# Optimization experiments

Measured on AMD Instinct MI355X. Metric: run time of the kernel, lower is better.

Reference implementation:

```python
import jax, jax.numpy as jnp
import numpy as np

S, B, D, H = 4096, 4, 1024, 16
DH = D // H


def _xavier(key, fan_in, fan_out):
    bound = float(np.sqrt(6.0 / (fan_in + fan_out)))
    return jax.random.uniform(key, (fan_out, fan_in), jnp.float32, -bound, bound)


def setup_inputs() -> dict:
    key = jax.random.key(0)
    kq, kk, kv, kwq, kwk, kwv = jax.random.split(key, 6)
    return {
        "q": jax.random.normal(kq, (S, B, D), jnp.float32),
        "k": jax.random.normal(kk, (S, B, D), jnp.float32),
        "v": jax.random.normal(kv, (S, B, D), jnp.float32),
        "Wq": _xavier(kwq, D, D),
        "Wk": _xavier(kwk, D, D),
        "Wv": _xavier(kwv, D, D),
    }


def reference(q, k, v, Wq, Wk, Wv):
    s, b = q.shape[:2]
    # exp feature maps after bias-free linear projections (nn.Linear: x @ W.T)
    q_h = jnp.exp(q @ Wq.T).reshape(s, b, H, DH)
    k_h = jnp.exp(k @ Wk.T).reshape(s, b, H, DH)
    v_h = (v @ Wv.T).reshape(s, b, H, DH)
    # original: einsum('sbnd,sbnde->sbne', q, k[...,None]*v[None...]) / same-with-ones
    # contract over d without materializing the (s,b,n,d,e) outer product
    qk = jnp.einsum('sbnd,sbnd->sbn', q_h, k_h)[..., None]  # (s,b,n,1)
    out = (qk * v_h) / qk                                   # (s,b,n,dh)
    out = out.reshape(s, b, D)
    return jnp.cumsum(out, axis=1)  # cumsum over dim=1 (batch), as in source
```

## Files before the change

### kernel.cpp

```cpp
#include <hip/hip_runtime.h>
#include <hip/hip_bf16.h>


typedef short s16x8 __attribute__((ext_vector_type(8)));
typedef float f32x4 __attribute__((ext_vector_type(4)));

constexpr int M_ = 16384, N_ = 1024, K_ = 1024;
constexpr int BM = 256, BN = 256, BK = 64;
constexpr int KT = K_ / BK;
constexpr int LDS_BUF = 65536;
constexpr size_t LDS_TOTAL = 131072;

static __device__ __forceinline__ unsigned cvtpk(float lo, float hi) {
  unsigned r;
  asm("v_cvt_pk_bf16_f32 %0, %1, %2" : "=v"(r) : "v"(lo), "v"(hi));
  return r;
}

__global__ __launch_bounds__(512, 2) void la_gemm_cumsum(
    const float* __restrict__ Vp,
    const float* __restrict__ Wp,
    float* __restrict__ out)
{
  extern __shared__ char lds[];

  const int tid  = threadIdx.x;
  const int lane = tid & 63;
  const int wave = tid >> 6;
  const int wr = wave >> 2;
  const int wc = wave & 3;

  const int gid = blockIdx.x;
  const int xcd = gid & 7;
  const int q   = gid >> 3;
  const int mt  = xcd * 8 + (q >> 2);
  const int nt  = q & 3;

  const int srow   = tid >> 3;
  const int schunk = tid & 7;
  const float* sAp = Vp + (size_t)(mt * 256 + srow) * K_ + schunk * 8;
  const float* sBp = Wp + (size_t)(nt * 256 + srow) * K_ + schunk * 8;
  const int wbyte = srow * 128 + ((schunk ^ (srow & 7)) << 4);

  const int basa0 = (wr * 128 + (lane & 15)) * 128 + (((lane >> 4) ^ (lane & 7)) << 4);
  const int basa1 = basa0 ^ 64;
  const int basb0 = (wc * 64 + (lane & 15)) * 128 + (((lane >> 4) ^ (lane & 7)) << 4);
  const int basb1 = basb0 ^ 64;

  f32x4 acc[8][4] = {};
  float4 sa[8], sb[8];

  auto loadset = [&](int kt) {
#pragma unroll
    for (int i = 0; i < 4; ++i) {
      const float* pa = sAp + kt * 64 + i * (64 * K_);
      const float* pb = sBp + kt * 64 + i * (64 * K_);
      sa[2 * i]     = *(const float4*)pa;
      sa[2 * i + 1] = *(const float4*)(pa + 4);
      sb[2 * i]     = *(const float4*)pb;
      sb[2 * i + 1] = *(const float4*)(pb + 4);
    }
  };

  auto cvtwrite = [&](int buf) {
    char* A = lds + buf * LDS_BUF;
    char* B = A + 32768;
#pragma unroll
    for (int i = 0; i < 4; ++i) {
      uint4 wa, wb;
      wa.x = cvtpk(sa[2*i].x,   sa[2*i].y);   wa.y = cvtpk(sa[2*i].z,   sa[2*i].w);
      wa.z = cvtpk(sa[2*i+1].x, sa[2*i+1].y); wa.w = cvtpk(sa[2*i+1].z, sa[2*i+1].w);
      wb.x = cvtpk(sb[2*i].x,   sb[2*i].y);   wb.y = cvtpk(sb[2*i].z,   sb[2*i].w);
      wb.z = cvtpk(sb[2*i+1].x, sb[2*i+1].y); wb.w = cvtpk(sb[2*i+1].z, sb[2*i+1].w);
      *(uint4*)(A + wbyte + i * 8192) = wa;
      *(uint4*)(B + wbyte + i * 8192) = wb;
    }
  };

  auto compute = [&](int buf) {
    const char* A = lds + buf * LDS_BUF;
    const char* B = A + 32768;
#pragma unroll
    for (int kk = 0; kk < 2; ++kk) {
      const int ba = kk ? basa1 : basa0;
      const int bb = kk ? basb1 : basb0;
      s16x8 bf[4];
#pragma unroll
      for (int n = 0; n < 4; ++n) bf[n] = *(const s16x8*)(B + bb + n * 2048);
#pragma unroll
      for (int mh = 0; mh < 2; ++mh) {
        s16x8 af[4];
#pragma unroll
        for (int m = 0; m < 4; ++m) af[m] = *(const s16x8*)(A + ba + (mh * 4 + m) * 2048);
        __builtin_amdgcn_s_setprio(1);
#pragma unroll
        for (int m = 0; m < 4; ++m)
#pragma unroll
          for (int n = 0; n < 4; ++n)
            acc[mh * 4 + m][n] =
                __builtin_amdgcn_mfma_f32_16x16x32_bf16(af[m], bf[n], acc[mh * 4 + m][n], 0, 0, 0);
        __builtin_amdgcn_s_setprio(0);
      }
    }
  };

  loadset(0);
  cvtwrite(0);
  __syncthreads();

  for (int kt = 0; kt < KT; ++kt) {
    const int cur = kt & 1;
    if (kt + 1 < KT) loadset(kt + 1);
    compute(cur);
    if (kt + 1 < KT) cvtwrite(cur ^ 1);
    __syncthreads();
  }

#pragma unroll
  for (int m = 0; m < 8; ++m) {
    const int row0 = mt * 256 + wr * 128 + m * 16 + ((lane >> 4) << 2);
#pragma unroll
    for (int n = 0; n < 4; ++n) {
      f32x4 a = acc[m][n];
      a.y += a.x;  a.z += a.y;  a.w += a.z;
      const int col = nt * 256 + wc * 64 + n * 16 + (lane & 15);
      out[(size_t)(row0 + 0) * N_ + col] = a.x;
      out[(size_t)(row0 + 1) * N_ + col] = a.y;
      out[(size_t)(row0 + 2) * N_ + col] = a.z;
      out[(size_t)(row0 + 3) * N_ + col] = a.w;
    }
  }
}

extern "C" void kernel_launch(void* const* d_in, const int* in_sizes, int n_in,
                              void* d_out, int out_size, void* d_ws, size_t ws_size,
                              hipStream_t stream) {
  const float* v  = (const float*)d_in[2];
  const float* Wv = (const float*)d_in[5];
  float* out = (float*)d_out;
  (void)d_ws; (void)ws_size; (void)in_sizes; (void)n_in; (void)out_size;

  static int attr_done = 0;
  hipFuncSetAttribute((const void*)la_gemm_cumsum,
                      hipFuncAttributeMaxDynamicSharedMemorySize, (int)LDS_TOTAL);
  (void)attr_done;

  la_gemm_cumsum<<<dim3(256), dim3(512), LDS_TOTAL, stream>>>(v, Wv, out);
}
```

Baseline: 50.25 us.

## Interleave global prefetch and LDS writes with MFMA phases using barrier gates

Splits each K-tile iteration into four phases. Each phase issues LDS fragment reads plus a slice of the next tile's global loads or bf16 conversion writes, then waits at a workgroup barrier before running 16 MFMAs. The intent is to spread memory traffic evenly across the compute so that global latency and LDS writes overlap with matrix math, instead of bunching all loads before compute and all writes after it. In exchange it adds several more s_barrier calls per iteration and forces lgkmcnt(0) waits, which could serialize the waves if the phases are not balanced.

```diff
diff --git a/kernel.cpp b/kernel.cpp
--- a/kernel.cpp
+++ b/kernel.cpp
@@ -43,77 +43,105 @@
   const int wbyte = srow * 128 + ((schunk ^ (srow & 7)) << 4);
 
   const int basa0 = (wr * 128 + (lane & 15)) * 128 + (((lane >> 4) ^ (lane & 7)) << 4);
-  const int basa1 = basa0 ^ 64;
   const int basb0 = (wc * 64 + (lane & 15)) * 128 + (((lane >> 4) ^ (lane & 7)) << 4);
-  const int basb1 = basb0 ^ 64;
 
   f32x4 acc[8][4] = {};
   float4 sa[8], sb[8];
 
-  auto loadset = [&](int kt) {
-#pragma unroll
-    for (int i = 0; i < 4; ++i) {
-      const float* pa = sAp + kt * 64 + i * (64 * K_);
-      const float* pb = sBp + kt * 64 + i * (64 * K_);
-      sa[2 * i]     = *(const float4*)pa;
-      sa[2 * i + 1] = *(const float4*)(pa + 4);
-      sb[2 * i]     = *(const float4*)pb;
-      sb[2 * i + 1] = *(const float4*)(pb + 4);
-    }
-  };
+#define LOADGRP(g, kt1) do {                                                  \
+    const float* pa_ = sAp + (kt1) * 64 + (g) * (64 * K_);                    \
+    const float* pb_ = sBp + (kt1) * 64 + (g) * (64 * K_);                    \
+    sa[2*(g)]   = *(const float4*)pa_;  sa[2*(g)+1] = *(const float4*)(pa_+4);\
+    sb[2*(g)]   = *(const float4*)pb_;  sb[2*(g)+1] = *(const float4*)(pb_+4);\
+  } while (0)
 
-  auto cvtwrite = [&](int buf) {
-    char* A = lds + buf * LDS_BUF;
-    char* B = A + 32768;
-#pragma unroll
-    for (int i = 0; i < 4; ++i) {
-      uint4 wa, wb;
-      wa.x = cvtpk(sa[2*i].x,   sa[2*i].y);   wa.y = cvtpk(sa[2*i].z,   sa[2*i].w);
-      wa.z = cvtpk(sa[2*i+1].x, sa[2*i+1].y); wa.w = cvtpk(sa[2*i+1].z, sa[2*i+1].w);
-      wb.x = cvtpk(sb[2*i].x,   sb[2*i].y);   wb.y = cvtpk(sb[2*i].z,   sb[2*i].w);
-      wb.z = cvtpk(sb[2*i+1].x, sb[2*i+1].y); wb.w = cvtpk(sb[2*i+1].z, sb[2*i+1].w);
-      *(uint4*)(A + wbyte + i * 8192) = wa;
-      *(uint4*)(B + wbyte + i * 8192) = wb;
-    }
-  };
+#define WRITEGRP(g, Aw, Bw) do {                                              \
+    uint4 wa_, wb_;                                                           \
+    wa_.x = cvtpk(sa[2*(g)].x,   sa[2*(g)].y);                                \
+    wa_.y = cvtpk(sa[2*(g)].z,   sa[2*(g)].w);                                \
+    wa_.z = cvtpk(sa[2*(g)+1].x, sa[2*(g)+1].y);                              \
+    wa_.w = cvtpk(sa[2*(g)+1].z, sa[2*(g)+1].w);                              \
+    wb_.x = cvtpk(sb[2*(g)].x,   sb[2*(g)].y);                                \
+    wb_.y = cvtpk(sb[2*(g)].z,   sb[2*(g)].w);                                \
+    wb_.z = cvtpk(sb[2*(g)+1].x, sb[2*(g)+1].y);                              \
+    wb_.w = cvtpk(sb[2*(g)+1].z, sb[2*(g)+1].w);                              \
+    *(uint4*)((Aw) + wbyte + (g) * 8192) = wa_;                               \
+    *(uint4*)((Bw) + wbyte + (g) * 8192) = wb_;                               \
+  } while (0)
 
-  auto compute = [&](int buf) {
-    const char* A = lds + buf * LDS_BUF;
-    const char* B = A + 32768;
-#pragma unroll
-    for (int kk = 0; kk < 2; ++kk) {
-      const int ba = kk ? basa1 : basa0;
-      const int bb = kk ? basb1 : basb0;
-      s16x8 bf[4];
-#pragma unroll
-      for (int n = 0; n < 4; ++n) bf[n] = *(const s16x8*)(B + bb + n * 2048);
-#pragma unroll
-      for (int mh = 0; mh < 2; ++mh) {
-        s16x8 af[4];
-#pragma unroll
-        for (int m = 0; m < 4; ++m) af[m] = *(const s16x8*)(A + ba + (mh * 4 + m) * 2048);
-        __builtin_amdgcn_s_setprio(1);
-#pragma unroll
-        for (int m = 0; m < 4; ++m)
-#pragma unroll
-          for (int n = 0; n < 4; ++n)
-            acc[mh * 4 + m][n] =
-                __builtin_amdgcn_mfma_f32_16x16x32_bf16(af[m], bf[n], acc[mh * 4 + m][n], 0, 0, 0);
-        __builtin_amdgcn_s_setprio(0);
-      }
-    }
-  };
+#define DSREAD_A(Abuf, kk, mh, af) do {                                       \
+    const int ba_ = basa0 ^ ((kk) ? 64 : 0);                                  \
+    _Pragma("unroll")                                                         \
+    for (int m_ = 0; m_ < 4; ++m_)                                            \
+      af[m_] = *(const s16x8*)((Abuf) + ba_ + ((mh)*4 + m_) * 2048);          \
+  } while (0)
 
-  loadset(0);
-  cvtwrite(0);
+#define DSREAD_B(Bbuf, kk, bf) do {                                           \
+    const int bb_ = basb0 ^ ((kk) ? 64 : 0);                                  \
+    _Pragma("unroll")                                                         \
+    for (int n_ = 0; n_ < 4; ++n_)                                            \
+      bf[n_] = *(const s16x8*)((Bbuf) + bb_ + n_ * 2048);                     \
+  } while (0)
+
+#define MFMA16(mh, af, bf) do {                                               \
+    __builtin_amdgcn_s_setprio(1);                                            \
+    _Pragma("unroll")                                                         \
+    for (int m_ = 0; m_ < 4; ++m_)                                            \
+      _Pragma("unroll")                                                       \
+      for (int n_ = 0; n_ < 4; ++n_)                                          \
+        acc[(mh)*4 + m_][n_] = __builtin_amdgcn_mfma_f32_16x16x32_bf16(       \
+            af[m_], bf[n_], acc[(mh)*4 + m_][n_], 0, 0, 0);                   \
+    __builtin_amdgcn_s_setprio(0);                                            \
+  } while (0)
+
+#define PHASE_GATE()                                                          \
+    __builtin_amdgcn_s_barrier();                                             \
+    asm volatile("s_waitcnt lgkmcnt(0)" ::: "memory");                        \
+    __builtin_amdgcn_sched_barrier(0);
+
+  LOADGRP(0, 0); LOADGRP(1, 0); LOADGRP(2, 0); LOADGRP(3, 0);
+  {
+    char* Aw = lds; char* Bw = lds + 32768;
+    WRITEGRP(0, Aw, Bw); WRITEGRP(1, Aw, Bw);
+    WRITEGRP(2, Aw, Bw); WRITEGRP(3, Aw, Bw);
+  }
   __syncthreads();
 
   for (int kt = 0; kt < KT; ++kt) {
     const int cur = kt & 1;
-    if (kt + 1 < KT) loadset(kt + 1);
-    compute(cur);
-    if (kt + 1 < KT) cvtwrite(cur ^ 1);
-    __syncthreads();
+    const char* A = lds + cur * LDS_BUF;
+    const char* B = A + 32768;
+    char* Aw = lds + (cur ^ 1) * LDS_BUF;
+    char* Bw = Aw + 32768;
+    const bool pf = (kt + 1 < KT);
+
+    s16x8 af[4], bf0[4], bf1[4];
+
+    DSREAD_B(B, 0, bf0);
+    DSREAD_A(A, 0, 0, af);
+    if (pf) { LOADGRP(0, kt + 1); LOADGRP(1, kt + 1); }
+    PHASE_GATE();
+    MFMA16(0, af, bf0);
+    __builtin_amdgcn_s_barrier();
+
+    DSREAD_A(A, 0, 1, af);
+    if (pf) { LOADGRP(2, kt + 1); LOADGRP(3, kt + 1); }
+    PHASE_GATE();
+    MFMA16(1, af, bf0);
+    __builtin_amdgcn_s_barrier();
+
+    DSREAD_B(B, 1, bf1);
+    DSREAD_A(A, 1, 0, af);
+    if (pf) { WRITEGRP(0, Aw, Bw); WRITEGRP(1, Aw, Bw); }
+    PHASE_GATE();
+    MFMA16(0, af, bf1);
+    __builtin_amdgcn_s_barrier();
+
+    DSREAD_A(A, 1, 1, af);
+    if (pf) { WRITEGRP(2, Aw, Bw); WRITEGRP(3, Aw, Bw); }
+    PHASE_GATE();
+    MFMA16(1, af, bf1);
+    __builtin_amdgcn_s_barrier();
   }
 
 #pragma unroll
@@ -130,6 +158,13 @@
       out[(size_t)(row0 + 3) * N_ + col] = a.w;
     }
   }
+
+#undef LOADGRP
+#undef WRITEGRP
+#undef DSREAD_A
+#undef DSREAD_B
+#undef MFMA16
+#undef PHASE_GATE
 }
 
 extern "C" void kernel_launch(void* const* d_in, const int* in_sizes, int n_in,
@@ -140,10 +175,8 @@
   float* out = (float*)d_out;
   (void)d_ws; (void)ws_size; (void)in_sizes; (void)n_in; (void)out_size;
 
-  static int attr_done = 0;
   hipFuncSetAttribute((const void*)la_gemm_cumsum,
                       hipFuncAttributeMaxDynamicSharedMemorySize, (int)LDS_TOTAL);
-  (void)attr_done;
 
   la_gemm_cumsum<<<dim3(256), dim3(512), LDS_TOTAL, stream>>>(v, Wv, out);
 }
```

Result: slower. 57.93 us (+15.3%).

## Pre-convert inputs to bf16 and stream tiles with global_load_lds pipeline

Applied to the files above, without the earlier changes.

Adds a separate conversion kernel that writes bf16 copies of v and Wv into workspace. The GEMM then loads those copies straight into LDS with global_load_lds, using a double-buffered schedule split into four phases with barrier gates. This removes register staging and the in-loop conversion work, at the cost of an extra kernel launch and an extra full pass over v through HBM. The old kernel is kept as a fallback for when the workspace is too small.

```diff
diff --git a/kernel.cpp b/kernel.cpp
--- a/kernel.cpp
+++ b/kernel.cpp
@@ -6,10 +6,9 @@
 typedef float f32x4 __attribute__((ext_vector_type(4)));
 
 constexpr int M_ = 16384, N_ = 1024, K_ = 1024;
-constexpr int BM = 256, BN = 256, BK = 64;
-constexpr int KT = K_ / BK;
-constexpr int LDS_BUF = 65536;
-constexpr size_t LDS_TOTAL = 131072;
+constexpr int KT = 16;
+constexpr size_t WS_WB   = 33554432;
+constexpr size_t WS_NEED = 35651584;
 
 static __device__ __forceinline__ unsigned cvtpk(float lo, float hi) {
   unsigned r;
@@ -17,103 +16,127 @@
   return r;
 }
 
-__global__ __launch_bounds__(512, 2) void la_gemm_cumsum(
-    const float* __restrict__ Vp,
-    const float* __restrict__ Wp,
-    float* __restrict__ out)
-{
+__global__ __launch_bounds__(256) void cvt_bf16(const float* __restrict__ v,
+                                                const float* __restrict__ w,
+                                                unsigned short* __restrict__ vb,
+                                                unsigned short* __restrict__ wb) {
+  const int gs = gridDim.x * blockDim.x;
+  const int t0 = blockIdx.x * blockDim.x + threadIdx.x;
+  for (int i = t0; i < (M_ * K_ / 4); i += gs) {
+    float4 x = ((const float4*)v)[i];
+    uint2 p; p.x = cvtpk(x.x, x.y); p.y = cvtpk(x.z, x.w);
+    ((uint2*)vb)[i] = p;
+  }
+  for (int i = t0; i < (N_ * K_ / 4); i += gs) {
+    float4 x = ((const float4*)w)[i];
+    uint2 p; p.x = cvtpk(x.x, x.y); p.y = cvtpk(x.z, x.w);
+    ((uint2*)wb)[i] = p;
+  }
+}
+
+#define GLL(srcp, ldsoff)                                                     \
+  __builtin_amdgcn_global_load_lds(                                           \
+      (__attribute__((address_space(1))) void*)(void*)(srcp),                 \
+      (__attribute__((address_space(3))) void*)(void*)(lds + (ldsoff)),       \
+      16, 0, 0)
+
+#define GATE()                                                                \
+  __builtin_amdgcn_s_barrier();                                               \
+  asm volatile("s_waitcnt lgkmcnt(0)" ::: "memory");                          \
+  __builtin_amdgcn_sched_barrier(0)
+
+#define MFMA_Q(MB, AF, BF)                                                    \
+  __builtin_amdgcn_s_setprio(1);                                              \
+  _Pragma("unroll") for (int m_ = 0; m_ < 4; ++m_)                            \
+  _Pragma("unroll") for (int n_ = 0; n_ < 4; ++n_)                            \
+      acc[(MB) + m_][n_] = __builtin_amdgcn_mfma_f32_16x16x32_bf16(           \
+          AF[m_], BF[n_], acc[(MB) + m_][n_], 0, 0, 0);                       \
+  __builtin_amdgcn_s_setprio(0);
+
+__global__ __launch_bounds__(512, 2) void la_gemm8(
+    const unsigned short* __restrict__ Ab,
+    const unsigned short* __restrict__ Bb,
+    float* __restrict__ out) {
   extern __shared__ char lds[];
 
-  const int tid  = threadIdx.x;
-  const int lane = tid & 63;
-  const int wave = tid >> 6;
-  const int wr = wave >> 2;
-  const int wc = wave & 3;
+  const int tid = threadIdx.x, lane = tid & 63, wave = tid >> 6;
+  const int wr = wave >> 2, wc = wave & 3;
 
   const int gid = blockIdx.x;
-  const int xcd = gid & 7;
-  const int q   = gid >> 3;
-  const int mt  = xcd * 8 + (q >> 2);
-  const int nt  = q & 3;
-
-  const int srow   = tid >> 3;
-  const int schunk = tid & 7;
-  const float* sAp = Vp + (size_t)(mt * 256 + srow) * K_ + schunk * 8;
-  const float* sBp = Wp + (size_t)(nt * 256 + srow) * K_ + schunk * 8;
-  const int wbyte = srow * 128 + ((schunk ^ (srow & 7)) << 4);
-
-  const int basa0 = (wr * 128 + (lane & 15)) * 128 + (((lane >> 4) ^ (lane & 7)) << 4);
-  const int basa1 = basa0 ^ 64;
-  const int basb0 = (wc * 64 + (lane & 15)) * 128 + (((lane >> 4) ^ (lane & 7)) << 4);
-  const int basb1 = basb0 ^ 64;
+  const int xcd = gid & 7, qq = gid >> 3;
+  const int mt = xcd * 8 + (qq >> 2), nt = qq & 3;
+
+  const int l3 = lane >> 3, l7 = lane & 7;
+  const int sch = ((l7 ^ l3) << 4);
+  const char* sA[2][2]; const char* sB[2][2];
+#pragma unroll
+  for (int h = 0; h < 2; ++h)
+#pragma unroll
+    for (int j = 0; j < 2; ++j) {
+      const size_t ar = (size_t)(mt * 256 + h * 128 + j * 64 + wave * 8 + l3);
+      const size_t br = (size_t)(nt * 256 + h * 128 + j * 64 + wave * 8 + l3);
+      sA[h][j] = (const char*)Ab + ar * 2048 + sch;
+      sB[h][j] = (const char*)Bb + br * 2048 + sch;
+    }
+  const int ldsw = wave * 1024;
+
+  const int basa = wr * 16384 + (lane & 15) * 128 + (((lane >> 4) ^ l7) << 4);
+  const int basb = 32768 + (wc >> 1) * 16384 +
+                   ((wc & 1) * 64 + (lane & 15)) * 128 + (((lane >> 4) ^ l7) << 4);
 
   f32x4 acc[8][4] = {};
-  float4 sa[8], sb[8];
-
-  auto loadset = [&](int kt) {
-#pragma unroll
-    for (int i = 0; i < 4; ++i) {
-      const float* pa = sAp + kt * 64 + i * (64 * K_);
-      const float* pb = sBp + kt * 64 + i * (64 * K_);
-      sa[2 * i]     = *(const float4*)pa;
-      sa[2 * i + 1] = *(const float4*)(pa + 4);
-      sb[2 * i]     = *(const float4*)pb;
-      sb[2 * i + 1] = *(const float4*)(pb + 4);
-    }
-  };
-
-  auto cvtwrite = [&](int buf) {
-    char* A = lds + buf * LDS_BUF;
-    char* B = A + 32768;
-#pragma unroll
-    for (int i = 0; i < 4; ++i) {
-      uint4 wa, wb;
-      wa.x = cvtpk(sa[2*i].x,   sa[2*i].y);   wa.y = cvtpk(sa[2*i].z,   sa[2*i].w);
-      wa.z = cvtpk(sa[2*i+1].x, sa[2*i+1].y); wa.w = cvtpk(sa[2*i+1].z, sa[2*i+1].w);
-      wb.x = cvtpk(sb[2*i].x,   sb[2*i].y);   wb.y = cvtpk(sb[2*i].z,   sb[2*i].w);
-      wb.z = cvtpk(sb[2*i+1].x, sb[2*i+1].y); wb.w = cvtpk(sb[2*i+1].z, sb[2*i+1].w);
-      *(uint4*)(A + wbyte + i * 8192) = wa;
-      *(uint4*)(B + wbyte + i * 8192) = wb;
-    }
-  };
-
-  auto compute = [&](int buf) {
-    const char* A = lds + buf * LDS_BUF;
-    const char* B = A + 32768;
-#pragma unroll
-    for (int kk = 0; kk < 2; ++kk) {
-      const int ba = kk ? basa1 : basa0;
-      const int bb = kk ? basb1 : basb0;
-      s16x8 bf[4];
-#pragma unroll
-      for (int n = 0; n < 4; ++n) bf[n] = *(const s16x8*)(B + bb + n * 2048);
-#pragma unroll
-      for (int mh = 0; mh < 2; ++mh) {
-        s16x8 af[4];
-#pragma unroll
-        for (int m = 0; m < 4; ++m) af[m] = *(const s16x8*)(A + ba + (mh * 4 + m) * 2048);
-        __builtin_amdgcn_s_setprio(1);
-#pragma unroll
-        for (int m = 0; m < 4; ++m)
-#pragma unroll
-          for (int n = 0; n < 4; ++n)
-            acc[mh * 4 + m][n] =
-                __builtin_amdgcn_mfma_f32_16x16x32_bf16(af[m], bf[n], acc[mh * 4 + m][n], 0, 0, 0);
-        __builtin_amdgcn_s_setprio(0);
-      }
-    }
-  };
-
-  loadset(0);
-  cvtwrite(0);
+
+  GLL(sA[0][0], 0 + ldsw);             GLL(sA[0][1], 8192 + ldsw);
+  GLL(sA[1][0], 16384 + ldsw);         GLL(sA[1][1], 24576 + ldsw);
+  GLL(sB[0][0], 32768 + ldsw);         GLL(sB[0][1], 40960 + ldsw);
+  GLL(sB[1][0], 49152 + ldsw);         GLL(sB[1][1], 57344 + ldsw);
+  asm volatile("s_waitcnt vmcnt(0)" ::: "memory");
   __syncthreads();
 
   for (int kt = 0; kt < KT; ++kt) {
-    const int cur = kt & 1;
-    if (kt + 1 < KT) loadset(kt + 1);
-    compute(cur);
-    if (kt + 1 < KT) cvtwrite(cur ^ 1);
-    __syncthreads();
+    const int cb = (kt & 1) << 16;
+    const int nb = cb ^ 65536;
+    const int ko = (kt + 1) * 128;
+    const bool pf = (kt + 1 < KT);
+
+    s16x8 af[4], ag[4], bf0[4], bf1[4];
+
+#pragma unroll
+    for (int n = 0; n < 4; ++n) bf0[n] = *(const s16x8*)(lds + cb + basb + n * 2048);
+#pragma unroll
+    for (int m = 0; m < 4; ++m) af[m] = *(const s16x8*)(lds + cb + basa + m * 2048);
+    if (pf) {
+      GLL(sA[0][0] + ko, nb + 0     + ldsw);  GLL(sA[0][1] + ko, nb + 8192  + ldsw);
+      GLL(sA[1][0] + ko, nb + 16384 + ldsw);  GLL(sA[1][1] + ko, nb + 24576 + ldsw);
+    }
+    GATE();
+    MFMA_Q(0, af, bf0);
+    __builtin_amdgcn_s_barrier();
+
+#pragma unroll
+    for (int m = 0; m < 4; ++m) ag[m] = *(const s16x8*)(lds + cb + basa + (4 + m) * 2048);
+    if (pf) {
+      GLL(sB[0][0] + ko, nb + 32768 + ldsw);  GLL(sB[0][1] + ko, nb + 40960 + ldsw);
+      GLL(sB[1][0] + ko, nb + 49152 + ldsw);  GLL(sB[1][1] + ko, nb + 57344 + ldsw);
+    }
+    GATE();
+    MFMA_Q(4, ag, bf0);
+    __builtin_amdgcn_s_barrier();
+
+#pragma unroll
+    for (int n = 0; n < 4; ++n) bf1[n] = *(const s16x8*)(lds + cb + ((basb + n * 2048) ^ 64));
+#pragma unroll
+    for (int m = 0; m < 4; ++m) af[m] = *(const s16x8*)(lds + cb + ((basa + m * 2048) ^ 64));
+    GATE();
+    MFMA_Q(0, af, bf1);
+    __builtin_amdgcn_s_barrier();
+
+#pragma unroll
+    for (int m = 0; m < 4; ++m) ag[m] = *(const s16x8*)(lds + cb + ((basa + (4 + m) * 2048) ^ 64));
+    GATE();
+    MFMA_Q(4, ag, bf1);
+    asm volatile("s_waitcnt vmcnt(0)" ::: "memory");
+    __builtin_amdgcn_s_barrier();
   }
 
 #pragma unroll
@@ -132,18 +155,108 @@
   }
 }
 
+__global__ __launch_bounds__(512, 2) void la_gemm_fb(
+    const float* __restrict__ Vp, const float* __restrict__ Wp, float* __restrict__ out) {
+  extern __shared__ char lds[];
+  const int tid = threadIdx.x, lane = tid & 63, wave = tid >> 6;
+  const int wr = wave >> 2, wc = wave & 3;
+  const int gid = blockIdx.x, xcd = gid & 7, q = gid >> 3;
+  const int mt = xcd * 8 + (q >> 2), nt = q & 3;
+  const int srow = tid >> 3, schunk = tid & 7;
+  const float* sAp = Vp + (size_t)(mt * 256 + srow) * K_ + schunk * 8;
+  const float* sBp = Wp + (size_t)(nt * 256 + srow) * K_ + schunk * 8;
+  const int wbyte = srow * 128 + ((schunk ^ (srow & 7)) << 4);
+  const int basa0 = (wr * 128 + (lane & 15)) * 128 + (((lane >> 4) ^ (lane & 7)) << 4);
+  const int basb0 = (wc * 64 + (lane & 15)) * 128 + (((lane >> 4) ^ (lane & 7)) << 4);
+  f32x4 acc[8][4] = {};
+  float4 sa[8], sb[8];
+  auto loadset = [&](int kt) {
+#pragma unroll
+    for (int i = 0; i < 4; ++i) {
+      const float* pa = sAp + kt * 64 + i * (64 * K_);
+      const float* pb = sBp + kt * 64 + i * (64 * K_);
+      sa[2*i] = *(const float4*)pa; sa[2*i+1] = *(const float4*)(pa + 4);
+      sb[2*i] = *(const float4*)pb; sb[2*i+1] = *(const float4*)(pb + 4);
+    }
+  };
+  auto cvtwrite = [&](int buf) {
+    char* A = lds + buf * 65536; char* B = A + 32768;
+#pragma unroll
+    for (int i = 0; i < 4; ++i) {
+      uint4 wa, wb;
+      wa.x = cvtpk(sa[2*i].x, sa[2*i].y);     wa.y = cvtpk(sa[2*i].z, sa[2*i].w);
+      wa.z = cvtpk(sa[2*i+1].x, sa[2*i+1].y); wa.w = cvtpk(sa[2*i+1].z, sa[2*i+1].w);
+      wb.x = cvtpk(sb[2*i].x, sb[2*i].y);     wb.y = cvtpk(sb[2*i].z, sb[2*i].w);
+      wb.z = cvtpk(sb[2*i+1].x, sb[2*i+1].y); wb.w = cvtpk(sb[2*i+1].z, sb[2*i+1].w);
+      *(uint4*)(A + wbyte + i * 8192) = wa;
+      *(uint4*)(B + wbyte + i * 8192) = wb;
+    }
+  };
+  auto compute = [&](int buf) {
+    const char* A = lds + buf * 65536; const char* B = A + 32768;
+#pragma unroll
+    for (int kk = 0; kk < 2; ++kk) {
+      const int ba = basa0 ^ (kk ? 64 : 0), bb = basb0 ^ (kk ? 64 : 0);
+      s16x8 bf[4];
+#pragma unroll
+      for (int n = 0; n < 4; ++n) bf[n] = *(const s16x8*)(B + bb + n * 2048);
+#pragma unroll
+      for (int mh = 0; mh < 2; ++mh) {
+        s16x8 af[4];
+#pragma unroll
+        for (int m = 0; m < 4; ++m) af[m] = *(const s16x8*)(A + ba + (mh * 4 + m) * 2048);
+        __builtin_amdgcn_s_setprio(1);
+#pragma unroll
+        for (int m = 0; m < 4; ++m)
+#pragma unroll
+          for (int n = 0; n < 4; ++n)
+            acc[mh*4+m][n] = __builtin_amdgcn_mfma_f32_16x16x32_bf16(af[m], bf[n], acc[mh*4+m][n], 0, 0, 0);
+        __builtin_amdgcn_s_setprio(0);
+      }
+    }
+  };
+  loadset(0); cvtwrite(0); __syncthreads();
+  for (int kt = 0; kt < KT; ++kt) {
+    const int cur = kt & 1;
+    if (kt + 1 < KT) loadset(kt + 1);
+    compute(cur);
+    if (kt + 1 < KT) cvtwrite(cur ^ 1);
+    __syncthreads();
+  }
+#pragma unroll
+  for (int m = 0; m < 8; ++m) {
+    const int row0 = mt * 256 + wr * 128 + m * 16 + ((lane >> 4) << 2);
+#pragma unroll
+    for (int n = 0; n < 4; ++n) {
+      f32x4 a = acc[m][n];
+      a.y += a.x; a.z += a.y; a.w += a.z;
+      const int col = nt * 256 + wc * 64 + n * 16 + (lane & 15);
+      out[(size_t)(row0 + 0) * N_ + col] = a.x;
+      out[(size_t)(row0 + 1) * N_ + col] = a.y;
+      out[(size_t)(row0 + 2) * N_ + col] = a.z;
+      out[(size_t)(row0 + 3) * N_ + col] = a.w;
+    }
+  }
+}
+
 extern "C" void kernel_launch(void* const* d_in, const int* in_sizes, int n_in,
                               void* d_out, int out_size, void* d_ws, size_t ws_size,
                               hipStream_t stream) {
   const float* v  = (const float*)d_in[2];
   const float* Wv = (const float*)d_in[5];
   float* out = (float*)d_out;
-  (void)d_ws; (void)ws_size; (void)in_sizes; (void)n_in; (void)out_size;
-
-  static int attr_done = 0;
-  hipFuncSetAttribute((const void*)la_gemm_cumsum,
-                      hipFuncAttributeMaxDynamicSharedMemorySize, (int)LDS_TOTAL);
-  (void)attr_done;
-
-  la_gemm_cumsum<<<dim3(256), dim3(512), LDS_TOTAL, stream>>>(v, Wv, out);
-}
+  (void)in_sizes; (void)n_in; (void)out_size;
+
+  if (ws_size >= WS_NEED) {
+    unsigned short* vb = (unsigned short*)d_ws;
+    unsigned short* wb = (unsigned short*)((char*)d_ws + WS_WB);
+    cvt_bf16<<<dim3(2048), dim3(256), 0, stream>>>(v, Wv, vb, wb);
+    hipFuncSetAttribute((const void*)la_gemm8,
+                        hipFuncAttributeMaxDynamicSharedMemorySize, 131072);
+    la_gemm8<<<dim3(256), dim3(512), 131072, stream>>>(vb, wb, out);
+  } else {
+    hipFuncSetAttribute((const void*)la_gemm_fb,
+                        hipFuncAttributeMaxDynamicSharedMemorySize, 131072);
+    la_gemm_fb<<<dim3(256), dim3(512), 131072, stream>>>(v, Wv, out);
+  }
+}
```

After: 58.59 us. +16.6%, slower.
